# Kernel optimization log

Measured on AMD Instinct MI355X. Metric: run time of the kernel, lower is better.

## Reference

```python
import jax, jax.numpy as jnp
import numpy as np

B, C, H, I = 32, 8, 512, 512


def act(x):
    # CustomActivation == hardtanh: (|x+1| - |x-1|) / 2
    return (jnp.abs(x + 1.0) - jnp.abs(x - 1.0)) * 0.5


def setup_inputs() -> dict:
    key = jax.random.key(0)
    ks = jax.random.split(key, 12)
    inp = jax.random.normal(ks[0], (B, C, H, I), dtype=jnp.float32)
    p_mask = jax.random.normal(ks[1], (H, I), dtype=jnp.float32)
    # Wp: tril(randn) with diagonal filled to 1 (matches __init__ + the no_grad
    # tril/clamp projection in forward, which is a no-op right after init).
    Wp = jnp.tril(jax.random.normal(ks[2], (H, H), dtype=jnp.float32))
    Wp = Wp - jnp.diag(jnp.diag(Wp)) + jnp.eye(H, dtype=jnp.float32)
    Wp_diag = jnp.ones((H,), dtype=jnp.float32)
    Wzp = jax.random.normal(ks[3], (H, H), dtype=jnp.float32)
    s = 1.0 / np.sqrt(I)
    def lin(k):
        kw, kb = jax.random.split(k)
        W = jax.random.uniform(kw, (I, I), jnp.float32, -s, s)
        b = jax.random.uniform(kb, (I,), jnp.float32, -s, s)
        return W, b
    p_lin_w, p_lin_b = lin(ks[4])
    z_lin_w, z_lin_b = lin(ks[5])
    fc1_w, fc1_b = lin(ks[6])
    fc2_w, fc2_b = lin(ks[7])
    return {
        'input': inp, 'p_mask': p_mask, 'Wp': Wp, 'Wp_diag': Wp_diag, 'Wzp': Wzp,
        'p_lin_w': p_lin_w, 'p_lin_b': p_lin_b,
        'z_lin_w': z_lin_w, 'z_lin_b': z_lin_b,
        'fc1_w': fc1_w, 'fc1_b': fc1_b, 'fc2_w': fc2_w, 'fc2_b': fc2_b,
    }


def reference(input, p_mask, Wp, Wp_diag, Wzp,
              p_lin_w, p_lin_b, z_lin_w, z_lin_b,
              fc1_w, fc1_b, fc2_w, fc2_b):
    x = input * (1.0 / 5000.0)                      # [B,C,H,I]
    p_set = x * act(p_mask)                         # split_input, broadcast over B,C
    Wp_eff = Wp + jnp.diag(Wp_diag)                 # [H,H]
    # per-channel Wp @ p_set[c], batched over B and C in one GEMM
    tp = jnp.einsum('hk,bcki->bchi', Wp_eff, p_set)
    tp = act(act(tp) @ p_lin_w.T + p_lin_b)         # p_output_layer
    tz = jnp.einsum('hk,bchi->bchi', Wzp, tp)       # wait-free channel-batched GEMM
    tz = act(act(tz) @ z_lin_w.T + z_lin_b)         # z_output_layer
    # sum over in_channel (out_channel==1 so broadcast-accumulate == sum)
    combined = tp.sum(axis=1) + tz.sum(axis=1) + x[:, 0]  # [B,H,I]
    out = jax.nn.relu(combined @ fc1_w.T + fc1_b)
    out = out @ fc2_w.T + fc2_b
    return out
```

## Files before the change

### kernel.cpp

```cpp
#include <hip/hip_runtime.h>

namespace {

constexpr int Bn = 32, Cn = 8, Hn = 512, In = 512;
constexpr size_t HI = (size_t)Hn * In;
constexpr float SC = 1.0f / 5000.0f;

using s16x8 = __attribute__((ext_vector_type(8))) short;
using f32x4 = __attribute__((ext_vector_type(4))) float;

__device__ __forceinline__ float actf(float x) {
    return fminf(1.0f, fmaxf(-1.0f, x));
}

__device__ __forceinline__ unsigned short f2bf(float f) {
    unsigned u = __builtin_bit_cast(unsigned, f);
    u += 0x7FFFu + ((u >> 16) & 1u);
    return (unsigned short)(u >> 16);
}
__device__ __forceinline__ float bf2f(unsigned short h) {
    return __builtin_bit_cast(float, (unsigned)h << 16);
}

__device__ __forceinline__ void async16(const void* g, void* l) {
    __builtin_amdgcn_global_load_lds(
        (const __attribute__((address_space(1))) unsigned*)g,
        (__attribute__((address_space(3))) unsigned*)l, 16, 0, 0);
}

template<int EPI, bool PCOL, bool TRI>
__global__ __launch_bounds__(256, 3) void mfma_gemm(
    const unsigned short* __restrict__ A,
    const unsigned short* __restrict__ Bt,
    const float* __restrict__ bias,
    const float* __restrict__ zrow,
    unsigned short* __restrict__ out0,
    unsigned short* __restrict__ out1,
    float* __restrict__ outf,
    size_t sB, size_t sC)
{
    __shared__ __align__(16) unsigned short As[128 * 32];
    __shared__ __align__(16) unsigned short Bs[128 * 32];

    const int tid  = threadIdx.x;
    const int wid  = tid >> 6, lane = tid & 63;
    const int wr   = wid >> 1, wc = wid & 1;
    const int l15  = lane & 15, kq = lane >> 4;

    const int bid = blockIdx.x;
    const int p = ((bid >> 5) << 3) | (bid & 7);
    const int q = (bid >> 3) & 3;
    const int rt = PCOL ? q : p;
    const int ct = PCOL ? (p & 3) : q;
    const size_t zb = PCOL ? (size_t)(p >> 2) : 0;

    const char* Ab = (const char*)A + (size_t)rt * 131072;
    const char* Bb = (const char*)(Bt + zb * sB) + (size_t)ct * 131072;

    f32x4 acc[4][4] = {};

    const int o0  = tid * 16;
    const int r0s = o0 >> 6;
    const int c0s = o0 & 63;
    const int csw = c0s ^ (((r0s >> 1) & 3) << 4);

    const int kSteps = TRI ? (rt + 1) * 4 : 16;

    for (int ks = 0; ks < kSteps; ++ks) {
        const int k0b = ks * 64;
        async16(Ab + (size_t)r0s * 1024 + k0b + csw,        (char*)As + wid * 1024);
        async16(Ab + (size_t)(64 + r0s) * 1024 + k0b + csw, (char*)As + 4096 + wid * 1024);
        async16(Bb + (size_t)r0s * 1024 + k0b + csw,        (char*)Bs + wid * 1024);
        async16(Bb + (size_t)(64 + r0s) * 1024 + k0b + csw, (char*)Bs + 4096 + wid * 1024);
        __syncthreads();

        s16x8 a[4], b[4];
        const int kx = kq * 16 ^ (((l15 >> 1) & 3) << 4);
        const int ar = wr * 64 + l15;
        const int br = wc * 64 + l15;
        #pragma unroll
        for (int m = 0; m < 4; ++m)
            a[m] = *(const s16x8*)((const char*)As + (size_t)(ar + m * 16) * 64 + kx);
        #pragma unroll
        for (int n = 0; n < 4; ++n)
            b[n] = *(const s16x8*)((const char*)Bs + (size_t)(br + n * 16) * 64 + kx);
        #pragma unroll
        for (int m = 0; m < 4; ++m)
            #pragma unroll
            for (int n = 0; n < 4; ++n)
                acc[m][n] = __builtin_amdgcn_mfma_f32_16x16x32_bf16(a[m], b[n], acc[m][n], 0, 0, 0);
        __syncthreads();
    }

    const int cb = ct * 128 + wc * 64 + l15;
    const int rb = rt * 128 + wr * 64 + (kq << 2);
    #pragma unroll
    for (int m = 0; m < 4; ++m) {
        #pragma unroll
        for (int n = 0; n < 4; ++n) {
            const int c = cb + n * 16;
            #pragma unroll
            for (int j = 0; j < 4; ++j) {
                const int r = rb + m * 16 + j;
                float v = acc[m][n][j];
                const size_t idx = zb * sC + (size_t)r * 512 + c;
                if (EPI == 0) {
                    out0[idx] = f2bf(actf(v));
                } else if (EPI == 1) {
                    float tp = actf(v + bias[c]);
                    out0[idx] = f2bf(tp);
                    out1[idx] = f2bf(actf(zrow[r & 511] * tp));
                } else if (EPI == 2) {
                    out0[idx] = f2bf(actf(v + bias[c]));
                } else if (EPI == 3) {
                    out0[idx] = f2bf(fmaxf(v + bias[c], 0.0f));
                } else {
                    outf[idx] = v + bias[c];
                }
            }
        }
    }
}

__global__ __launch_bounds__(256) void reduce_both(
    const unsigned short* __restrict__ tp,
    const unsigned short* __restrict__ tz,
    const float* __restrict__ x0,
    unsigned short* __restrict__ comb)
{
    size_t idx = (size_t)blockIdx.x * 256 + threadIdx.x;
    size_t b = idx >> 16;
    size_t p = (idx & 65535) * 4;
    float4 xv = *(const float4*)&x0[(b * Cn) * HI + p];
    float s0 = xv.x * SC, s1 = xv.y * SC, s2 = xv.z * SC, s3 = xv.w * SC;
    #pragma unroll
    for (int c = 0; c < Cn; ++c) {
        size_t q = (b * Cn + c) * HI + p;
        ushort4 a = *(const ushort4*)&tp[q];
        ushort4 d = *(const ushort4*)&tz[q];
        s0 += bf2f(a.x) + bf2f(d.x);
        s1 += bf2f(a.y) + bf2f(d.y);
        s2 += bf2f(a.z) + bf2f(d.z);
        s3 += bf2f(a.w) + bf2f(d.w);
    }
    ushort4 o;
    o.x = f2bf(s0); o.y = f2bf(s1); o.z = f2bf(s2); o.w = f2bf(s3);
    *(ushort4*)&comb[b * HI + p] = o;
}

__global__ __launch_bounds__(256) void transpose_mask(
    const float* __restrict__ x, const float* __restrict__ mask,
    unsigned short* __restrict__ xst)
{
    __shared__ float t[64][65];
    const int bc = blockIdx.z;
    const int i0 = blockIdx.x * 64, k0 = blockIdx.y * 64;
    const int r4 = threadIdx.x >> 6, cc = threadIdx.x & 63;
    const float* xp = x + (size_t)bc * HI;
    #pragma unroll
    for (int it = 0; it < 16; ++it) {
        int kl = it * 4 + r4;
        size_t g = (size_t)(k0 + kl) * In + i0 + cc;
        t[kl][cc] = xp[g] * (actf(mask[g]) * SC);
    }
    __syncthreads();
    unsigned short* op = xst + (size_t)bc * HI;
    #pragma unroll
    for (int it = 0; it < 16; ++it) {
        int il = it * 4 + r4;
        op[(size_t)(i0 + il) * Hn + k0 + cc] = f2bf(t[cc][il]);
    }
}

__global__ __launch_bounds__(256) void prep_wpe_bf(
    const float* __restrict__ Wp, const float* __restrict__ Wpd,
    unsigned short* __restrict__ o)
{
    int idx = blockIdx.x * 256 + threadIdx.x;
    int i = idx >> 9, j = idx & 511;
    o[idx] = f2bf(Wp[idx] + (i == j ? Wpd[i] : 0.0f));
}

__global__ __launch_bounds__(256) void conv_bf(
    const float* __restrict__ s, unsigned short* __restrict__ o)
{
    int idx = blockIdx.x * 256 + threadIdx.x;
    o[idx] = f2bf(s[idx]);
}

__global__ __launch_bounds__(64) void rowsum(
    const float* __restrict__ W, float* __restrict__ zr)
{
    int h = blockIdx.x, l = threadIdx.x;
    float s = 0.0f;
    for (int k = l; k < Hn; k += 64) s += W[h * Hn + k];
    #pragma unroll
    for (int off = 32; off; off >>= 1) s += __shfl_down(s, off, 64);
    if (!l) zr[h] = s;
}

}

extern "C" void kernel_launch(void* const* d_in, const int* in_sizes, int n_in,
                              void* d_out, int out_size, void* d_ws, size_t ws_size,
                              hipStream_t stream)
{
    const float* input  = (const float*)d_in[0];
    const float* p_mask = (const float*)d_in[1];
    const float* Wp     = (const float*)d_in[2];
    const float* Wpd    = (const float*)d_in[3];
    const float* Wzp    = (const float*)d_in[4];
    const float* plw    = (const float*)d_in[5];
    const float* plb    = (const float*)d_in[6];
    const float* zlw    = (const float*)d_in[7];
    const float* zlb    = (const float*)d_in[8];
    const float* f1w    = (const float*)d_in[9];
    const float* f1b    = (const float*)d_in[10];
    const float* f2w    = (const float*)d_in[11];
    const float* f2b    = (const float*)d_in[12];

    constexpr size_t WB = 512 * 512 * 2;
    char* w = (char*)d_ws;
    auto alloc = [&](size_t bytes) { char* p = w; w += (bytes + 255) & ~255ull; return p; };

    unsigned short* Wpeb  = (unsigned short*)alloc(WB);
    unsigned short* plwb  = (unsigned short*)alloc(WB);
    unsigned short* zlwb  = (unsigned short*)alloc(WB);
    unsigned short* f1wb  = (unsigned short*)alloc(WB);
    unsigned short* f2wb  = (unsigned short*)alloc(WB);
    float*          zrw   = (float*)alloc(512 * 4);
    unsigned short* combb = (unsigned short*)alloc((size_t)Bn * HI * 2);
    unsigned short* out1  = (unsigned short*)alloc((size_t)Bn * HI * 2);

    size_t fixedB = (size_t)(w - (char*)d_ws);
    int chunk = 32;
    while (chunk > 1 &&
           fixedB + 4ull * (size_t)chunk * Cn * HI * 2 + 4096 > ws_size)
        chunk >>= 1;
    const size_t CB = (size_t)chunk * Cn * HI * 2;
    unsigned short* xst   = (unsigned short*)alloc(CB);
    unsigned short* tpact = (unsigned short*)alloc(CB);
    unsigned short* tpb   = (unsigned short*)alloc(CB);
    unsigned short* tzin  = (unsigned short*)alloc(CB);
    unsigned short* tzb   = xst;

    prep_wpe_bf<<<512 * 512 / 256, 256, 0, stream>>>(Wp, Wpd, Wpeb);
    conv_bf<<<1024, 256, 0, stream>>>(plw, plwb);
    conv_bf<<<1024, 256, 0, stream>>>(zlw, zlwb);
    conv_bf<<<1024, 256, 0, stream>>>(f1w, f1wb);
    conv_bf<<<1024, 256, 0, stream>>>(f2w, f2wb);
    rowsum<<<512, 64, 0, stream>>>(Wzp, zrw);

    for (int b0 = 0; b0 < Bn; b0 += chunk) {
        const int nc = chunk * Cn;
        const float* inp_c = input + (size_t)b0 * Cn * HI;

        transpose_mask<<<dim3(8, 8, nc), 256, 0, stream>>>(inp_c, p_mask, xst);
        mfma_gemm<0, true, true><<<nc * 16, 256, 0, stream>>>(
            Wpeb, xst, nullptr, nullptr, tpact, nullptr, nullptr, HI, HI);
        mfma_gemm<1, false, false><<<nc * 16, 256, 0, stream>>>(
            tpact, plwb, plb, zrw, tpb, tzin, nullptr, 0, 0);
        mfma_gemm<2, false, false><<<nc * 16, 256, 0, stream>>>(
            tzin, zlwb, zlb, nullptr, tzb, nullptr, nullptr, 0, 0);
        reduce_both<<<chunk * 256, 256, 0, stream>>>(
            tpb, tzb, inp_c, combb + (size_t)b0 * HI);
    }

    mfma_gemm<3, false, false><<<512, 256, 0, stream>>>(
        combb, f1wb, f1b, nullptr, out1, nullptr, nullptr, 0, 0);
    mfma_gemm<4, false, false><<<512, 256, 0, stream>>>(
        out1, f2wb, f2b, nullptr, nullptr, nullptr, (float*)d_out, 0, 0);
}
```

Measured before the change: 560.1 us.

## Double-buffer LDS tiles in MFMA GEMM to overlap async loads with compute

Replaces the single-buffered A/B LDS tiles with two 16 KB buffers. The main loop now prefetches the next K-step through async global-to-LDS loads while computing on the other buffer, using explicit vmcnt waits and barriers. The goal is to hide global-load latency that the old load-sync-compute-sync loop exposed. LDS use per block doubles, which may reduce occupancy under the 3-blocks-per-CU bound. Correctness depends on kSteps always being even and on the vmcnt counting being right.

```diff
diff --git a/kernel.cpp b/kernel.cpp
--- a/kernel.cpp
+++ b/kernel.cpp
@@ -27,6 +27,8 @@
         (const __attribute__((address_space(1))) unsigned*)g,
         (__attribute__((address_space(3))) unsigned*)l, 16, 0, 0);
 }
+
+#define CFENCE asm volatile("" ::: "memory")
 
 template<int EPI, bool PCOL, bool TRI>
 __global__ __launch_bounds__(256, 3) void mfma_gemm(
@@ -39,8 +41,7 @@
     float* __restrict__ outf,
     size_t sB, size_t sC)
 {
-    __shared__ __align__(16) unsigned short As[128 * 32];
-    __shared__ __align__(16) unsigned short Bs[128 * 32];
+    __shared__ __align__(16) char lds[2][16384];
 
     const int tid  = threadIdx.x;
     const int wid  = tid >> 6, lane = tid & 63;
@@ -64,32 +65,49 @@
     const int c0s = o0 & 63;
     const int csw = c0s ^ (((r0s >> 1) & 3) << 4);
 
-    const int kSteps = TRI ? (rt + 1) * 4 : 16;
-
-    for (int ks = 0; ks < kSteps; ++ks) {
-        const int k0b = ks * 64;
-        async16(Ab + (size_t)r0s * 1024 + k0b + csw,        (char*)As + wid * 1024);
-        async16(Ab + (size_t)(64 + r0s) * 1024 + k0b + csw, (char*)As + 4096 + wid * 1024);
-        async16(Bb + (size_t)r0s * 1024 + k0b + csw,        (char*)Bs + wid * 1024);
-        async16(Bb + (size_t)(64 + r0s) * 1024 + k0b + csw, (char*)Bs + 4096 + wid * 1024);
-        __syncthreads();
-
+    auto stage = [&](char* buf, int k0b) {
+        async16(Ab + (size_t)r0s * 1024 + k0b + csw,        buf + wid * 1024);
+        async16(Ab + (size_t)(64 + r0s) * 1024 + k0b + csw, buf + 4096 + wid * 1024);
+        async16(Bb + (size_t)r0s * 1024 + k0b + csw,        buf + 8192 + wid * 1024);
+        async16(Bb + (size_t)(64 + r0s) * 1024 + k0b + csw, buf + 12288 + wid * 1024);
+    };
+    auto compute = [&](const char* buf) {
         s16x8 a[4], b[4];
         const int kx = kq * 16 ^ (((l15 >> 1) & 3) << 4);
         const int ar = wr * 64 + l15;
         const int br = wc * 64 + l15;
         #pragma unroll
         for (int m = 0; m < 4; ++m)
-            a[m] = *(const s16x8*)((const char*)As + (size_t)(ar + m * 16) * 64 + kx);
+            a[m] = *(const s16x8*)(buf + (size_t)(ar + m * 16) * 64 + kx);
         #pragma unroll
         for (int n = 0; n < 4; ++n)
-            b[n] = *(const s16x8*)((const char*)Bs + (size_t)(br + n * 16) * 64 + kx);
+            b[n] = *(const s16x8*)(buf + 8192 + (size_t)(br + n * 16) * 64 + kx);
         #pragma unroll
         for (int m = 0; m < 4; ++m)
             #pragma unroll
             for (int n = 0; n < 4; ++n)
                 acc[m][n] = __builtin_amdgcn_mfma_f32_16x16x32_bf16(a[m], b[n], acc[m][n], 0, 0, 0);
-        __syncthreads();
+    };
+
+    const int kSteps = TRI ? (rt + 1) * 4 : 16;
+
+    stage(lds[0], 0);
+    stage(lds[1], 64);
+
+    #pragma unroll 1
+    for (int ks = 0; ks < kSteps; ks += 2) {
+        const bool more = (ks + 2 < kSteps);
+        asm volatile("s_waitcnt vmcnt(4)" ::: "memory");
+        __builtin_amdgcn_s_barrier(); CFENCE;
+        compute(lds[0]);
+        CFENCE; __builtin_amdgcn_s_barrier();
+        if (more) stage(lds[0], (ks + 2) * 64);
+        if (more) asm volatile("s_waitcnt vmcnt(4)" ::: "memory");
+        else      asm volatile("s_waitcnt vmcnt(0)" ::: "memory");
+        __builtin_amdgcn_s_barrier(); CFENCE;
+        compute(lds[1]);
+        CFENCE; __builtin_amdgcn_s_barrier();
+        if (more) stage(lds[1], (ks + 3) * 64);
     }
 
     const int cb = ct * 128 + wc * 64 + l15;
```

After: 555.9 us. About the same (-0.7%).

## Double-buffer per-wave private LDS tiles and drop block-wide barriers in GEMM loop

Applied to the files above, without the earlier changes.

Each wave now loads its own 64-row A and B slices into a private double-buffered LDS region and prefetches two k-steps ahead, using vmcnt/lgkmcnt waits in place of __syncthreads. This is meant to overlap global-to-LDS loads with MFMA work and remove block-level synchronization stalls. The cost is that A and B tiles are duplicated across waves (each wave loads rows other waves also need), which raises global traffic and LDS use to 64KB per block. Occupancy is lowered to 2 blocks per CU.

```diff
diff --git a/kernel.cpp b/kernel.cpp
--- a/kernel.cpp
+++ b/kernel.cpp
@@ -29,7 +29,7 @@
 }
 
 template<int EPI, bool PCOL, bool TRI>
-__global__ __launch_bounds__(256, 3) void mfma_gemm(
+__global__ __launch_bounds__(256, 2) void mfma_gemm(
     const unsigned short* __restrict__ A,
     const unsigned short* __restrict__ Bt,
     const float* __restrict__ bias,
@@ -39,8 +39,7 @@
     float* __restrict__ outf,
     size_t sB, size_t sC)
 {
-    __shared__ __align__(16) unsigned short As[128 * 32];
-    __shared__ __align__(16) unsigned short Bs[128 * 32];
+    __shared__ __align__(16) char lds[4][2][8192];
 
     const int tid  = threadIdx.x;
     const int wid  = tid >> 6, lane = tid & 63;
@@ -54,42 +53,59 @@
     const int ct = PCOL ? (p & 3) : q;
     const size_t zb = PCOL ? (size_t)(p >> 2) : 0;
 
-    const char* Ab = (const char*)A + (size_t)rt * 131072;
-    const char* Bb = (const char*)(Bt + zb * sB) + (size_t)ct * 131072;
+    const char* Aw = (const char*)A + ((size_t)rt * 128 + wr * 64) * 1024;
+    const char* Bw = (const char*)(Bt + zb * sB) + ((size_t)ct * 128 + wc * 64) * 1024;
 
     f32x4 acc[4][4] = {};
 
-    const int o0  = tid * 16;
-    const int r0s = o0 >> 6;
-    const int c0s = o0 & 63;
-    const int csw = c0s ^ (((r0s >> 1) & 3) << 4);
-
-    const int kSteps = TRI ? (rt + 1) * 4 : 16;
-
-    for (int ks = 0; ks < kSteps; ++ks) {
-        const int k0b = ks * 64;
-        async16(Ab + (size_t)r0s * 1024 + k0b + csw,        (char*)As + wid * 1024);
-        async16(Ab + (size_t)(64 + r0s) * 1024 + k0b + csw, (char*)As + 4096 + wid * 1024);
-        async16(Bb + (size_t)r0s * 1024 + k0b + csw,        (char*)Bs + wid * 1024);
-        async16(Bb + (size_t)(64 + r0s) * 1024 + k0b + csw, (char*)Bs + 4096 + wid * 1024);
-        __syncthreads();
-
+    const int srow = lane >> 2;
+    const int csw  = ((lane & 3) * 16) ^ (((lane >> 3) & 3) << 4);
+    char* myl = &lds[wid][0][0];
+
+    auto stage = [&](int buf, int k0b) {
+        char* d = myl + buf * 8192;
+        const char* Ag = Aw + k0b + csw;
+        const char* Bg = Bw + k0b + csw;
+        #pragma unroll
+        for (int i = 0; i < 4; ++i)
+            async16(Ag + (size_t)(srow + 16 * i) * 1024, d + i * 1024 + lane * 16);
+        #pragma unroll
+        for (int i = 0; i < 4; ++i)
+            async16(Bg + (size_t)(srow + 16 * i) * 1024, d + 4096 + i * 1024 + lane * 16);
+    };
+    auto compute = [&](int buf) {
+        const char* pp = myl + buf * 8192;
         s16x8 a[4], b[4];
         const int kx = kq * 16 ^ (((l15 >> 1) & 3) << 4);
-        const int ar = wr * 64 + l15;
-        const int br = wc * 64 + l15;
         #pragma unroll
         for (int m = 0; m < 4; ++m)
-            a[m] = *(const s16x8*)((const char*)As + (size_t)(ar + m * 16) * 64 + kx);
+            a[m] = *(const s16x8*)(pp + (size_t)(m * 16 + l15) * 64 + kx);
         #pragma unroll
         for (int n = 0; n < 4; ++n)
-            b[n] = *(const s16x8*)((const char*)Bs + (size_t)(br + n * 16) * 64 + kx);
+            b[n] = *(const s16x8*)(pp + 4096 + (size_t)(n * 16 + l15) * 64 + kx);
         #pragma unroll
         for (int m = 0; m < 4; ++m)
             #pragma unroll
             for (int n = 0; n < 4; ++n)
                 acc[m][n] = __builtin_amdgcn_mfma_f32_16x16x32_bf16(a[m], b[n], acc[m][n], 0, 0, 0);
-        __syncthreads();
+    };
+
+    const int kSteps = TRI ? (rt + 1) * 4 : 16;
+
+    stage(0, 0);
+    stage(1, 64);
+
+    #pragma unroll 1
+    for (int ks = 0; ks < kSteps; ++ks) {
+        if (ks + 1 < kSteps)
+            asm volatile("s_waitcnt vmcnt(8)" ::: "memory");
+        else
+            asm volatile("s_waitcnt vmcnt(0)" ::: "memory");
+        compute(ks & 1);
+        if (ks + 2 < kSteps) {
+            asm volatile("s_waitcnt lgkmcnt(0)" ::: "memory");
+            stage(ks & 1, (ks + 2) * 64);
+        }
     }
 
     const int cb = ct * 128 + wc * 64 + l15;
```

Result: slower. 647.8 us (+15.7%).
